# Kernel tuning notes

Hardware: AMD Instinct MI355X
Metric: run time of the kernel (lower is better)

The kernel has to match this reference:

```python
import jax, jax.numpy as jnp
import numpy as np

N, E, F, HID, PC, HEADS = 100000, 1600000, 128, 128, 16, 4
RATIO = 0.8
NEG_SLOPE = 0.2
BIG_NEG = -1e9


def setup_inputs() -> dict:
    ks = jax.random.split(jax.random.key(0), 20)
    def g(k, shape, fan):
        return jax.random.normal(k, shape, jnp.float32) / np.float32(np.sqrt(fan))
    return {
        "x": jax.random.normal(ks[0], (N, F), jnp.float32),
        "edge_index": jax.random.randint(ks[1], (2, E), 0, N, dtype=jnp.int32),
        "edge_attr": jax.random.uniform(ks[2], (E, 1), dtype=jnp.float32),
        "W1": g(ks[3], (F, PC), F),
        "att_src1": g(ks[4], (HEADS, PC // HEADS), PC // HEADS),
        "att_dst1": g(ks[5], (HEADS, PC // HEADS), PC // HEADS),
        "We1": g(ks[6], (1, PC), 1),
        "att_edge1": g(ks[7], (HEADS, PC // HEADS), PC // HEADS),
        "b1": jnp.zeros((PC,), jnp.float32),
        "Wrel": g(ks[8], (PC, 1), PC),
        "brel": jnp.zeros((1,), jnp.float32),
        "Wroot": g(ks[9], (PC, 1), PC),
        "W2": g(ks[10], (PC, HID), PC),
        "att_src2": g(ks[11], (1, HID), HID),
        "att_dst2": g(ks[12], (1, HID), HID),
        "We2": g(ks[13], (1, HID), 1),
        "att_edge2": g(ks[14], (1, HID), HID),
        "b2": jnp.zeros((HID,), jnp.float32),
        "Wg": g(ks[15], (HID, 1), HID),
        "bg": jnp.zeros((1,), jnp.float32),
    }


def gat_conv(h_in, src, dst, e_attr, W, a_s, a_d, We, a_e, b, num_nodes, mask=None):
    """PyG GATConv (add_self_loops=False, eval-mode so dropout is identity)."""
    H, D = a_s.shape
    h = (h_in @ W).reshape(-1, H, D)                      # [N,H,D]
    al_s = jnp.einsum('nhd,hd->nh', h, a_s)               # alpha contribution of source
    al_d = jnp.einsum('nhd,hd->nh', h, a_d)               # alpha contribution of dest
    he = (e_attr @ We).reshape(-1, H, D)                  # [E,H,D] edge features
    al_e = jnp.einsum('ehd,hd->eh', he, a_e)              # [E,H]
    logits = jax.nn.leaky_relu(al_s[src] + al_d[dst] + al_e, NEG_SLOPE)  # [E,H]
    if mask is not None:
        logits = jnp.where(mask[:, None], logits, BIG_NEG)
    # segment softmax over incoming edges of each destination node
    m = jnp.maximum(jax.ops.segment_max(logits, dst, num_segments=num_nodes), BIG_NEG)
    num = jnp.exp(logits - m[dst])
    if mask is not None:
        num = jnp.where(mask[:, None], num, 0.0)
    den = jax.ops.segment_sum(num, dst, num_segments=num_nodes)
    coef = num / jnp.maximum(den[dst], 1e-16)             # [E,H]
    out = jax.ops.segment_sum(coef[:, :, None] * h[src], dst, num_segments=num_nodes)
    return out.reshape(num_nodes, H * D) + b


def _forward(x, edge_attr, W1, att_src1, att_dst1, We1, att_edge1, b1,
             Wrel, brel, Wroot, W2, att_src2, att_dst2, We2, att_edge2, b2,
             Wg, bg, edge_index):
    n = x.shape[0]
    src, dst = edge_index[0], edge_index[1]
    h1 = jax.nn.relu(gat_conv(x, src, dst, edge_attr, W1, att_src1, att_dst1, We1, att_edge1, b1, n))
    # --- SAGPooling: GraphConv score -> tanh -> top-k -> masked subgraph (n > node_threshold always) ---
    agg = jax.ops.segment_sum(h1[src], dst, num_segments=n)           # neighbor sum
    score = (agg @ Wrel + brel + h1 @ Wroot).reshape(-1)              # GraphConv(16 -> 1)
    k = int(np.ceil(RATIO * n))                                       # static
    vals, perm = jax.lax.top_k(score, k)
    new_idx = jnp.full((n,), -1, dtype=jnp.int32).at[perm].set(jnp.arange(k, dtype=jnp.int32))
    src_n, dst_n = new_idx[src], new_idx[dst]
    emask = (src_n >= 0) & (dst_n >= 0)                               # edges with both ends kept
    src2 = jnp.where(emask, src_n, 0)
    dst2 = jnp.where(emask, dst_n, 0)
    x2 = h1[perm] * jnp.tanh(vals)[:, None]                           # gate kept nodes
    h2 = jax.nn.relu(gat_conv(x2, src2, dst2, edge_attr, W2, att_src2, att_dst2, We2, att_edge2, b2, k, mask=emask))
    # --- AttentionalAggregation + MaxAggregation over the single graph (index = zeros) ---
    gate = jax.nn.softmax(h2 @ Wg + bg, axis=0)                       # [k,1]
    att = (gate * h2).sum(axis=0, keepdims=True)                      # [1,HID]
    mx = h2.max(axis=0, keepdims=True)                                # [1,HID]
    return jnp.concatenate([att, mx], axis=1)                         # [1,2*HID]


def reference(x, edge_index, edge_attr, W1, att_src1, att_dst1, We1, att_edge1, b1,
              Wrel, brel, Wroot, W2, att_src2, att_dst2, We2, att_edge2, b2, Wg, bg):
    return _forward(x, edge_attr, W1, att_src1, att_dst1, We1, att_edge1, b1,
                    Wrel, brel, Wroot, W2, att_src2, att_dst2, We2, att_edge2, b2,
                    Wg, bg, edge_index)
```

## Files before the change

kernel.cpp:

```cpp
#include <hip/hip_runtime.h>
#include <hip/hip_bf16.h>

#define Nn 100000
#define Ee 1600000
#define Kk 80000
#define NB ((Nn + 255) / 256)
#define NBK 196
#define CHK 8192
#define G2B 2048

typedef unsigned int uint;
typedef unsigned short ushort;

struct Scal {
    uint prefix, remaining, needEq;
    float c1[4];
    float c2;
    uint gmaxOrd;
    float deng;
    float attnum[128];
    uint mxOrd[128];
};

__device__ __forceinline__ uint f2ord(float f) {
    uint b = __float_as_uint(f);
    return (b & 0x80000000u) ? ~b : (b | 0x80000000u);
}
__device__ __forceinline__ float ord2f(uint u) {
    uint b = (u & 0x80000000u) ? (u ^ 0x80000000u) : ~u;
    return __uint_as_float(b);
}
__device__ __forceinline__ float lrelu(float v) { return v > 0.f ? v : 0.2f * v; }
__device__ __forceinline__ float2 bf2f2(uint u) {
    return make_float2(__uint_as_float(u << 16), __uint_as_float(u & 0xFFFF0000u));
}

__global__ __launch_bounds__(256) void initK(uint* bcnt, uint* hist, Scal* sc,
                                             const float* We1, const float* ae1,
                                             const float* We2, const float* ae2) {
    int i = blockIdx.x * 256 + threadIdx.x;
    if (i < NBK) bcnt[i] = 0u;
    if (i < 256) hist[i] = 0u;
    if (i == 0) {
        sc->prefix = 0u; sc->remaining = Kk; sc->needEq = 0u;
        for (int h = 0; h < 4; h++) {
            float s = 0.f;
            for (int d = 0; d < 4; d++) s += We1[h * 4 + d] * ae1[h * 4 + d];
            sc->c1[h] = s;
        }
        float s2 = 0.f;
        for (int d = 0; d < 128; d++) s2 += We2[d] * ae2[d];
        sc->c2 = s2;
    }
}

__global__ __launch_bounds__(256) void nodeL1(const float* __restrict__ x,
                                              const float* __restrict__ W1,
                                              const float* __restrict__ as1,
                                              const float* __restrict__ ad1,
                                              float* __restrict__ hpre,
                                              float* __restrict__ alS1,
                                              float* __restrict__ alD1) {
    __shared__ float Ws[128 * 16];
    __shared__ float s_as[16], s_ad[16];
    for (int i = threadIdx.x; i < 2048; i += 256) Ws[i] = W1[i];
    if (threadIdx.x < 16) { s_as[threadIdx.x] = as1[threadIdx.x]; s_ad[threadIdx.x] = ad1[threadIdx.x]; }
    __syncthreads();
    int n = blockIdx.x * 256 + threadIdx.x;
    if (n >= Nn) return;
    float acc[16];
#pragma unroll
    for (int j = 0; j < 16; j++) acc[j] = 0.f;
    const float4* xr = (const float4*)(x + (size_t)n * 128);
    for (int t4 = 0; t4 < 32; t4++) {
        float4 xv = xr[t4];
#pragma unroll
        for (int j = 0; j < 16; j++) {
            acc[j] += xv.x * Ws[(t4 * 4 + 0) * 16 + j];
            acc[j] += xv.y * Ws[(t4 * 4 + 1) * 16 + j];
            acc[j] += xv.z * Ws[(t4 * 4 + 2) * 16 + j];
            acc[j] += xv.w * Ws[(t4 * 4 + 3) * 16 + j];
        }
    }
    float* hp = hpre + (size_t)n * 16;
#pragma unroll
    for (int j = 0; j < 16; j++) hp[j] = acc[j];
#pragma unroll
    for (int h = 0; h < 4; h++) {
        float s = 0.f, d = 0.f;
#pragma unroll
        for (int q = 0; q < 4; q++) {
            s += acc[h * 4 + q] * s_as[h * 4 + q];
            d += acc[h * 4 + q] * s_ad[h * 4 + q];
        }
        alS1[n * 4 + h] = s;
        alD1[n * 4 + h] = d;
    }
}

__global__ __launch_bounds__(256) void bucketCnt(const int* __restrict__ ei, uint* __restrict__ bcnt) {
    __shared__ uint h[NBK];
    if (threadIdx.x < NBK) h[threadIdx.x] = 0u;
    __syncthreads();
    for (int e = blockIdx.x * 256 + threadIdx.x; e < Ee; e += gridDim.x * 256)
        atomicAdd(&h[((uint)ei[Ee + e]) >> 9], 1u);
    __syncthreads();
    if (threadIdx.x < NBK && h[threadIdx.x]) atomicAdd(&bcnt[threadIdx.x], h[threadIdx.x]);
}

__global__ __launch_bounds__(256) void scanBk(const uint* __restrict__ bcnt, uint* __restrict__ boff,
                                              uint* __restrict__ gcur) {
    __shared__ uint s[256];
    int t = threadIdx.x;
    uint v = (t < NBK) ? bcnt[t] : 0u;
    s[t] = v;
    __syncthreads();
    for (int off = 1; off < 256; off <<= 1) {
        uint u = (t >= off) ? s[t - off] : 0u;
        __syncthreads();
        s[t] += u;
        __syncthreads();
    }
    if (t < NBK) { boff[t] = s[t] - v; gcur[t] = 0u; }
    if (t == 0) boff[NBK] = Ee;
}

__global__ __launch_bounds__(256) void binScat(const int* __restrict__ ei, const float* __restrict__ ea,
                                               const uint* __restrict__ boff, uint* __restrict__ gcur,
                                               uint2* __restrict__ bsE, ushort* __restrict__ bsD) {
    __shared__ uint h[NBK], base[NBK], h2[NBK];
    int t = threadIdx.x;
    if (t < NBK) h[t] = 0u;
    __syncthreads();
    int estart = blockIdx.x * CHK;
    int eend = min(Ee, estart + CHK);
    for (int e = estart + t; e < eend; e += 256)
        atomicAdd(&h[((uint)ei[Ee + e]) >> 9], 1u);
    __syncthreads();
    if (t < NBK) { base[t] = atomicAdd(&gcur[t], h[t]); h2[t] = 0u; }
    __syncthreads();
    for (int e = estart + t; e < eend; e += 256) {
        uint d = (uint)ei[Ee + e];
        uint b = d >> 9;
        uint r = atomicAdd(&h2[b], 1u);
        uint pos = boff[b] + base[b] + r;
        bsE[pos] = make_uint2((uint)ei[e], __float_as_uint(ea[e]));
        bsD[pos] = (ushort)(d & 511u);
    }
}

__global__ __launch_bounds__(256) void rankPlace(const uint* __restrict__ boff, const uint2* __restrict__ bsE,
                                                 const ushort* __restrict__ bsD,
                                                 uint2* __restrict__ csr_p8, uint* __restrict__ rowstart) {
    __shared__ uint ldeg[512];
    __shared__ uint lscan[512];
    __shared__ uint ps[256];
    int b = blockIdx.x, t = threadIdx.x;
    ldeg[t] = 0u; ldeg[t + 256] = 0u;
    __syncthreads();
    uint r0 = boff[b], r1 = boff[b + 1];
    for (uint i = r0 + t; i < r1; i += 256)
        atomicAdd(&ldeg[bsD[i]], 1u);
    __syncthreads();
    uint pv = ldeg[2 * t] + ldeg[2 * t + 1];
    ps[t] = pv;
    __syncthreads();
    for (int off = 1; off < 256; off <<= 1) {
        uint u = (t >= off) ? ps[t - off] : 0u;
        __syncthreads();
        ps[t] += u;
        __syncthreads();
    }
    uint pbase = ps[t] - pv;
    lscan[2 * t] = pbase;
    lscan[2 * t + 1] = pbase + ldeg[2 * t];
    __syncthreads();
    uint bb = boff[b];
    int nd = b * 512 + t;
    if (nd < Nn) rowstart[nd] = bb + lscan[t];
    nd = b * 512 + 256 + t;
    if (nd < Nn) rowstart[nd] = bb + lscan[256 + t];
    if (b == 0 && t == 0) rowstart[Nn] = Ee;
    ldeg[t] = 0u; ldeg[t + 256] = 0u;
    __syncthreads();
    for (uint i = r0 + t; i < r1; i += 256) {
        ushort dl = bsD[i];
        uint r = atomicAdd(&ldeg[dl], 1u);
        csr_p8[bb + lscan[dl] + r] = bsE[i];
    }
}

__global__ __launch_bounds__(256) void gather1f(const uint2* __restrict__ csr_p8,
                                                const uint* __restrict__ rowstart,
                                                const float* __restrict__ alS1, const float* __restrict__ alD1,
                                                const float* __restrict__ hpre, const Scal* __restrict__ scc,
                                                const float* __restrict__ b1, const float* __restrict__ Wrel,
                                                const float* __restrict__ Wroot,
                                                float* __restrict__ h1, float* __restrict__ p,
                                                float* __restrict__ q) {
    int tid = blockIdx.x * 256 + threadIdx.x;
    if (tid >= Nn * 4) return;
    int d = tid >> 2, h = tid & 3;
    uint r0 = rowstart[d], r1 = rowstart[d + 1];
    float ad = alD1[tid];
    float c1h = scc->c1[h];
    float den = 0.f;
    float4 acc = {0.f, 0.f, 0.f, 0.f};
#pragma unroll 8
    for (uint i = r0; i < r1; i++) {
        uint2 p8 = csr_p8[i];
        int s = (int)p8.x;
        float e = __expf(lrelu(alS1[s * 4 + h] + __uint_as_float(p8.y) * c1h + ad));
        float4 hv = *(const float4*)(hpre + (size_t)s * 16 + h * 4);
        den += e;
        acc.x += e * hv.x; acc.y += e * hv.y;
        acc.z += e * hv.z; acc.w += e * hv.w;
    }
    float inv = 1.f / fmaxf(den, 1e-16f);
    float4 o;
    o.x = fmaxf(acc.x * inv + b1[h * 4 + 0], 0.f);
    o.y = fmaxf(acc.y * inv + b1[h * 4 + 1], 0.f);
    o.z = fmaxf(acc.z * inv + b1[h * 4 + 2], 0.f);
    o.w = fmaxf(acc.w * inv + b1[h * 4 + 3], 0.f);
    *(float4*)(h1 + (size_t)d * 16 + h * 4) = o;
    float pp = o.x * Wrel[h * 4 + 0] + o.y * Wrel[h * 4 + 1] + o.z * Wrel[h * 4 + 2] + o.w * Wrel[h * 4 + 3];
    float qq = o.x * Wroot[h * 4 + 0] + o.y * Wroot[h * 4 + 1] + o.z * Wroot[h * 4 + 2] + o.w * Wroot[h * 4 + 3];
    pp += __shfl_xor(pp, 1); pp += __shfl_xor(pp, 2);
    qq += __shfl_xor(qq, 1); qq += __shfl_xor(qq, 2);
    if (h == 0) { p[d] = pp; q[d] = qq; }
}

__global__ __launch_bounds__(256) void scoreH(const uint2* __restrict__ csr_p8, const uint* __restrict__ rowstart,
                                              const float* __restrict__ p, const float* __restrict__ q,
                                              const float* __restrict__ brel,
                                              float* __restrict__ score, uint* __restrict__ dkey,
                                              uint* __restrict__ hist) {
    __shared__ uint lh[256];
    lh[threadIdx.x] = 0u;
    __syncthreads();
    int d = blockIdx.x * 256 + threadIdx.x;
    if (d < Nn) {
        uint r0 = rowstart[d], r1 = rowstart[d + 1];
        float s = brel[0] + q[d];
#pragma unroll 8
        for (uint i = r0; i < r1; i++) s += p[(int)csr_p8[i].x];
        score[d] = s;
        uint k = ~f2ord(s);
        dkey[d] = k;
        atomicAdd(&lh[k >> 24], 1u);
    }
    __syncthreads();
    if (lh[threadIdx.x]) atomicAdd(&hist[threadIdx.x], lh[threadIdx.x]);
}

__global__ __launch_bounds__(256) void histK(const uint* __restrict__ dkey, const Scal* __restrict__ sc,
                                             uint* __restrict__ hist, int shift) {
    __shared__ uint lh[256];
    lh[threadIdx.x] = 0u;
    __syncthreads();
    int i = blockIdx.x * 256 + threadIdx.x;
    if (i < Nn) {
        uint d = dkey[i];
        if ((d >> (shift + 8)) == sc->prefix) atomicAdd(&lh[(d >> shift) & 255u], 1u);
    }
    __syncthreads();
    if (lh[threadIdx.x]) atomicAdd(&hist[threadIdx.x], lh[threadIdx.x]);
}

__global__ __launch_bounds__(256) void selP(Scal* sc, uint* hist) {
    __shared__ uint s[256];
    int t = threadIdx.x;
    uint c = hist[t];
    s[t] = c;
    __syncthreads();
    for (int off = 1; off < 256; off <<= 1) {
        uint v = (t >= off) ? s[t - off] : 0u;
        __syncthreads();
        s[t] += v;
        __syncthreads();
    }
    uint rem = sc->remaining;
    uint cum = s[t];
    uint cumex = cum - c;
    if (cum >= rem && cumex < rem) {
        sc->remaining = rem - cumex;
        sc->prefix = (sc->prefix << 8) | (uint)t;
    }
    hist[t] = 0u;
}

__global__ __launch_bounds__(256) void cntK(const uint* __restrict__ dkey, const Scal* __restrict__ sc,
                                            uint* __restrict__ blkLt, uint* __restrict__ blkEq) {
    int i = blockIdx.x * 256 + threadIdx.x;
    uint ut = sc->prefix;
    bool lt = (i < Nn) && (dkey[i] < ut);
    bool eq = (i < Nn) && (dkey[i] == ut);
    __shared__ uint sl[4], se[4];
    unsigned long long bl = __ballot(lt), be = __ballot(eq);
    int lane = threadIdx.x & 63, w = threadIdx.x >> 6;
    if (lane == 0) { sl[w] = (uint)__popcll(bl); se[w] = (uint)__popcll(be); }
    __syncthreads();
    if (threadIdx.x == 0) {
        blkLt[blockIdx.x] = sl[0] + sl[1] + sl[2] + sl[3];
        blkEq[blockIdx.x] = se[0] + se[1] + se[2] + se[3];
    }
}

__global__ __launch_bounds__(512) void prefP(Scal* sc, const uint* __restrict__ blkLt,
                                             const uint* __restrict__ blkEq, uint* __restrict__ eqPref) {
    __shared__ uint se[512];
    __shared__ uint sl[512];
    int t = threadIdx.x;
    uint e = (t < NB) ? blkEq[t] : 0u;
    uint l = (t < NB) ? blkLt[t] : 0u;
    se[t] = e; sl[t] = l;
    __syncthreads();
    for (int off = 1; off < 512; off <<= 1) {
        uint v1 = (t >= off) ? se[t - off] : 0u;
        uint v2 = (t >= off) ? sl[t - off] : 0u;
        __syncthreads();
        se[t] += v1; sl[t] += v2;
        __syncthreads();
    }
    if (t < NB) eqPref[t] = se[t] - e;
    if (t == 511) sc->needEq = Kk - sl[511];
}

__global__ __launch_bounds__(256) void keptK(const uint* __restrict__ dkey, const Scal* __restrict__ sc,
                                             const uint* __restrict__ eqPref, int* __restrict__ kept) {
    int i = blockIdx.x * 256 + threadIdx.x;
    uint ut = sc->prefix, needEq = sc->needEq;
    bool inr = i < Nn;
    uint d = inr ? dkey[i] : 0xFFFFFFFFu;
    bool isLt = inr && (d < ut);
    bool isEq = inr && (d == ut);
    __shared__ uint wcnt[4];
    unsigned long long mask = __ballot(isEq);
    int lane = threadIdx.x & 63, w = threadIdx.x >> 6;
    uint lanePre = (uint)__popcll(mask & ((1ull << lane) - 1ull));
    if (lane == 0) wcnt[w] = (uint)__popcll(mask);
    __syncthreads();
    uint wo = 0;
    for (int qq = 0; qq < 4; qq++) if (qq < w) wo += wcnt[qq];
    uint rank = eqPref[blockIdx.x] + wo + lanePre;
    if (inr) kept[i] = (isLt || (isEq && rank < needEq)) ? 1 : 0;
}

__global__ __launch_bounds__(256) void nodeL2(const float* __restrict__ h1, const float* __restrict__ score,
                                              const int* __restrict__ kept, const float* __restrict__ W2,
                                              const float* __restrict__ as2, const float* __restrict__ ad2,
                                              __hip_bfloat162* __restrict__ h2b, float* __restrict__ alS2k,
                                              float* __restrict__ alD2) {
    __shared__ float Ws[16 * 128];
    for (int i = threadIdx.x; i < 2048; i += 256) Ws[i] = W2[i];
    __syncthreads();
    int wid = (blockIdx.x * 256 + threadIdx.x) >> 6;
    int lane = threadIdx.x & 63;
    if (wid >= Nn) return;
    int n = wid;
    if (!kept[n]) { if (lane == 0) alS2k[n] = -1e30f; return; }
    float t = tanhf(score[n]);
    float x2[16];
    const float* hr = h1 + (size_t)n * 16;
#pragma unroll
    for (int j = 0; j < 16; j++) x2[j] = hr[j] * t;
    int d0 = 2 * lane, d1 = 2 * lane + 1;
    float a0 = 0.f, a1 = 0.f;
    const float2* Wv = (const float2*)Ws;
#pragma unroll
    for (int j = 0; j < 16; j++) {
        float2 wv = Wv[j * 64 + lane];
        a0 += x2[j] * wv.x;
        a1 += x2[j] * wv.y;
    }
    __hip_bfloat162 hb;
    hb.x = __float2bfloat16(a0);
    hb.y = __float2bfloat16(a1);
    h2b[(size_t)n * 64 + lane] = hb;
    float s = a0 * as2[d0] + a1 * as2[d1];
    float dd = a0 * ad2[d0] + a1 * ad2[d1];
#pragma unroll
    for (int off = 32; off; off >>= 1) { s += __shfl_xor(s, off); dd += __shfl_xor(dd, off); }
    if (lane == 0) { alS2k[n] = s; alD2[n] = dd; }
}

__global__ __launch_bounds__(256) void gather2h(const uint2* __restrict__ csr_p8,
                                                const uint* __restrict__ rowstart,
                                                const float* __restrict__ alS2k, const float* __restrict__ alD2,
                                                const Scal* __restrict__ scc,
                                                const __hip_bfloat162* __restrict__ h2b, const float* __restrict__ b2,
                                                const float* __restrict__ Wg, const float* __restrict__ bg,
                                                float* __restrict__ pacc, float* __restrict__ pmx,
                                                float* __restrict__ pden) {
    __shared__ float sAtt[4][16][8];
    __shared__ float sMx[4][16][8];
    __shared__ float sDen[4];
    int w = threadIdx.x >> 6, lane = threadIdx.x & 63;
    int g = lane >> 4, t = lane & 15;
    float4 b2a = ((const float4*)b2)[t * 2], b2b = ((const float4*)b2)[t * 2 + 1];
    float4 wga = ((const float4*)Wg)[t * 2], wgb = ((const float4*)Wg)[t * 2 + 1];
    float bg0 = bg[0];
    float c2 = scc->c2;
    const uint* h2u = (const uint*)h2b;
    float att[8], mx8[8], denP = 0.f;
#pragma unroll
    for (int j = 0; j < 8; j++) { att[j] = 0.f; mx8[j] = 0.f; }
    for (int n = blockIdx.x * 4 + w; n < Nn; n += G2B * 4) {
        float sk = alS2k[n];
        if (sk <= -1e29f) continue;
        float ad = alD2[n];
        uint r0 = rowstart[n];
        uint len = rowstart[n + 1] - r0;
        float den = 0.f;
        float acc[8];
#pragma unroll
        for (int d = 0; d < 8; d++) acc[d] = 0.f;
#pragma unroll 2
        for (uint base = 0; base < len; base += 4) {
            float cmy = 0.f;
            int smy = 0;
            if (lane < 4) {
                uint off = base + (uint)lane;
                if (off < len) {
                    uint2 p8 = csr_p8[r0 + off];
                    smy = (int)p8.x;
                    float pv = alS2k[smy] + __uint_as_float(p8.y) * c2;
                    cmy = __expf(lrelu(pv + ad));
                }
            }
            float c = __shfl(cmy, g);
            int s = __shfl(smy, g);
            uint4 hv = *(const uint4*)(h2u + (size_t)s * 64 + t * 4);
            den += c;
            float2 f;
            f = bf2f2(hv.x); acc[0] += c * f.x; acc[1] += c * f.y;
            f = bf2f2(hv.y); acc[2] += c * f.x; acc[3] += c * f.y;
            f = bf2f2(hv.z); acc[4] += c * f.x; acc[5] += c * f.y;
            f = bf2f2(hv.w); acc[6] += c * f.x; acc[7] += c * f.y;
        }
#pragma unroll
        for (int d = 0; d < 8; d++) {
            acc[d] += __shfl_xor(acc[d], 16);
            acc[d] += __shfl_xor(acc[d], 32);
        }
        den += __shfl_xor(den, 16);
        den += __shfl_xor(den, 32);
        float inv = 1.f / fmaxf(den, 1e-16f);
        float o[8];
        o[0] = fmaxf(acc[0] * inv + b2a.x, 0.f);
        o[1] = fmaxf(acc[1] * inv + b2a.y, 0.f);
        o[2] = fmaxf(acc[2] * inv + b2a.z, 0.f);
        o[3] = fmaxf(acc[3] * inv + b2a.w, 0.f);
        o[4] = fmaxf(acc[4] * inv + b2b.x, 0.f);
        o[5] = fmaxf(acc[5] * inv + b2b.y, 0.f);
        o[6] = fmaxf(acc[6] * inv + b2b.z, 0.f);
        o[7] = fmaxf(acc[7] * inv + b2b.w, 0.f);
        float gp = o[0] * wga.x + o[1] * wga.y + o[2] * wga.z + o[3] * wga.w +
                   o[4] * wgb.x + o[5] * wgb.y + o[6] * wgb.z + o[7] * wgb.w;
#pragma unroll
        for (int off = 8; off; off >>= 1) gp += __shfl_xor(gp, off);
        float e = __expf(gp + bg0);
        denP += e;
#pragma unroll
        for (int j = 0; j < 8; j++) {
            att[j] += e * o[j];
            mx8[j] = fmaxf(mx8[j], o[j]);
        }
    }
    if (g == 0) {
#pragma unroll
        for (int j = 0; j < 8; j++) { sAtt[w][t][j] = att[j]; sMx[w][t][j] = mx8[j]; }
    }
    if (lane == 0) sDen[w] = denP;
    __syncthreads();
    int tid = threadIdx.x;
    if (tid < 128) {
        int tt = tid >> 3, j = tid & 7;
        float a = sAtt[0][tt][j] + sAtt[1][tt][j] + sAtt[2][tt][j] + sAtt[3][tt][j];
        float m = fmaxf(fmaxf(sMx[0][tt][j], sMx[1][tt][j]), fmaxf(sMx[2][tt][j], sMx[3][tt][j]));
        pacc[(size_t)blockIdx.x * 128 + tid] = a;
        pmx[(size_t)blockIdx.x * 128 + tid] = m;
    }
    if (tid == 0) pden[blockIdx.x] = sDen[0] + sDen[1] + sDen[2] + sDen[3];
}

__global__ __launch_bounds__(256) void gateOut(const float* __restrict__ pacc, const float* __restrict__ pmx,
                                               const float* __restrict__ pden, float* __restrict__ out) {
    __shared__ float r[256];
    __shared__ float rd[256];
    int b = blockIdx.x, tid = threadIdx.x;
    float a = 0.f, m = 0.f, dsum = 0.f;
    for (int i = tid; i < G2B; i += 256) {
        a += pacc[(size_t)i * 128 + b];
        m = fmaxf(m, pmx[(size_t)i * 128 + b]);
        dsum += pden[i];
    }
    r[tid] = a; rd[tid] = dsum;
    __syncthreads();
    for (int off = 128; off; off >>= 1) {
        if (tid < off) { r[tid] += r[tid + off]; rd[tid] += rd[tid + off]; }
        __syncthreads();
    }
    float asum = r[0], deng = rd[0];
    __syncthreads();
    r[tid] = m;
    __syncthreads();
    for (int off = 128; off; off >>= 1) {
        if (tid < off) r[tid] = fmaxf(r[tid], r[tid + off]);
        __syncthreads();
    }
    if (tid == 0) {
        out[b] = asum / deng;
        out[128 + b] = r[0];
    }
}

extern "C" void kernel_launch(void* const* d_in, const int* in_sizes, int n_in,
                              void* d_out, int out_size, void* d_ws, size_t ws_size,
                              hipStream_t stream) {
    const float* x = (const float*)d_in[0];
    const int* ei = (const int*)d_in[1];
    const float* ea = (const float*)d_in[2];
    const float* W1 = (const float*)d_in[3];
    const float* as1 = (const float*)d_in[4];
    const float* ad1 = (const float*)d_in[5];
    const float* We1 = (const float*)d_in[6];
    const float* ae1 = (const float*)d_in[7];
    const float* b1 = (const float*)d_in[8];
    const float* Wrel = (const float*)d_in[9];
    const float* brel = (const float*)d_in[10];
    const float* Wroot = (const float*)d_in[11];
    const float* W2 = (const float*)d_in[12];
    const float* as2 = (const float*)d_in[13];
    const float* ad2 = (const float*)d_in[14];
    const float* We2 = (const float*)d_in[15];
    const float* ae2 = (const float*)d_in[16];
    const float* b2 = (const float*)d_in[17];
    const float* Wg = (const float*)d_in[18];
    const float* bg = (const float*)d_in[19];
    float* out = (float*)d_out;

    float* base = (float*)d_ws;
    size_t o = 0;
    auto alloc = [&](size_t nf) { float* p2 = base + o; o += nf; return p2; };
    uint2* bsE = (uint2*)alloc((size_t)Ee * 2);
    ushort* bsD = (ushort*)alloc((size_t)Ee / 2);
    uint2* csr_p8 = (uint2*)alloc((size_t)Ee * 2);
    __hip_bfloat162* h2b = (__hip_bfloat162*)alloc((size_t)Nn * 64);
    float* hpre = alloc((size_t)Nn * 16);
    float* h1 = alloc((size_t)Nn * 16);
    float* pacc = alloc((size_t)G2B * 128);
    float* pmx = alloc((size_t)G2B * 128);
    float* pden = alloc(G2B);
    float* alS1 = alloc((size_t)Nn * 4);
    float* alD1 = alloc((size_t)Nn * 4);
    float* p = alloc(Nn);
    float* q = alloc(Nn);
    float* score = alloc(Nn);
    uint* dkey = (uint*)alloc(Nn);
    int* kept = (int*)alloc(Nn);
    float* alS2k = alloc(Nn);
    float* alD2 = alloc(Nn);
    uint* rowstart = (uint*)alloc(Nn + 1);
    uint* hist = (uint*)alloc(256);
    uint* blkLt = (uint*)alloc(NB);
    uint* blkEq = (uint*)alloc(NB);
    uint* eqPref = (uint*)alloc(NB);
    uint* bcnt = (uint*)alloc(NBK);
    uint* boff = (uint*)alloc(NBK + 1);
    uint* gcur = (uint*)alloc(NBK);
    Scal* sc = (Scal*)alloc(512);

    auto cdiv = [](long a, long b) { return (int)((a + b - 1) / b); };

    initK<<<NB, 256, 0, stream>>>(bcnt, hist, sc, We1, ae1, We2, ae2);
    nodeL1<<<NB, 256, 0, stream>>>(x, W1, as1, ad1, hpre, alS1, alD1);
    bucketCnt<<<512, 256, 0, stream>>>(ei, bcnt);
    scanBk<<<1, 256, 0, stream>>>(bcnt, boff, gcur);
    binScat<<<cdiv(Ee, CHK), 256, 0, stream>>>(ei, ea, boff, gcur, bsE, bsD);
    rankPlace<<<NBK, 256, 0, stream>>>(boff, bsE, bsD, csr_p8, rowstart);
    gather1f<<<cdiv((long)Nn * 4, 256), 256, 0, stream>>>(csr_p8, rowstart, alS1, alD1, hpre, sc,
                                                          b1, Wrel, Wroot, h1, p, q);
    scoreH<<<NB, 256, 0, stream>>>(csr_p8, rowstart, p, q, brel, score, dkey, hist);
    selP<<<1, 256, 0, stream>>>(sc, hist);
    for (int shift = 16; shift >= 0; shift -= 8) {
        histK<<<NB, 256, 0, stream>>>(dkey, sc, hist, shift);
        selP<<<1, 256, 0, stream>>>(sc, hist);
    }
    cntK<<<NB, 256, 0, stream>>>(dkey, sc, blkLt, blkEq);
    prefP<<<1, 512, 0, stream>>>(sc, blkLt, blkEq, eqPref);
    keptK<<<NB, 256, 0, stream>>>(dkey, sc, eqPref, kept);
    nodeL2<<<cdiv(Nn, 4), 256, 0, stream>>>(h1, score, kept, W2, as2, ad2, h2b, alS2k, alD2);
    gather2h<<<G2B, 256, 0, stream>>>(csr_p8, rowstart, alS2k, alD2, sc,
                                      h2b, b2, Wg, bg, pacc, pmx, pden);
    gateOut<<<128, 256, 0, stream>>>(pacc, pmx, pden, out);
}
```

Measured before the change: 335.5 us.

## Fuse radix top-k selection into one single-block kernel; compute edge weights per group in gather2

Replaces the chain of histogram, select, count, prefix and keep kernels for top-k with one 1024-thread single-block kernel. That kernel runs three more radix passes over all node keys and then a sequential ranked scan to mark kept nodes. This removes about ten kernel launches and their global round-trips, but a single workgroup now streams 100k keys four times. Separately, gather2 now has every lane compute its group's edge coefficient directly instead of four lanes computing and shuffling, and the unroll goes from 2 to 4.

```diff
diff --git a/kernel.cpp b/kernel.cpp
--- a/kernel.cpp
+++ b/kernel.cpp
@@ -13,22 +13,13 @@
 typedef unsigned short ushort;
 
 struct Scal {
-    uint prefix, remaining, needEq;
     float c1[4];
     float c2;
-    uint gmaxOrd;
-    float deng;
-    float attnum[128];
-    uint mxOrd[128];
 };
 
 __device__ __forceinline__ uint f2ord(float f) {
     uint b = __float_as_uint(f);
     return (b & 0x80000000u) ? ~b : (b | 0x80000000u);
-}
-__device__ __forceinline__ float ord2f(uint u) {
-    uint b = (u & 0x80000000u) ? (u ^ 0x80000000u) : ~u;
-    return __uint_as_float(b);
 }
 __device__ __forceinline__ float lrelu(float v) { return v > 0.f ? v : 0.2f * v; }
 __device__ __forceinline__ float2 bf2f2(uint u) {
@@ -42,7 +33,6 @@
     if (i < NBK) bcnt[i] = 0u;
     if (i < 256) hist[i] = 0u;
     if (i == 0) {
-        sc->prefix = 0u; sc->remaining = Kk; sc->needEq = 0u;
         for (int h = 0; h < 4; h++) {
             float s = 0.f;
             for (int d = 0; d < 4; d++) s += We1[h * 4 + d] * ae1[h * 4 + d];
@@ -253,97 +243,68 @@
     if (lh[threadIdx.x]) atomicAdd(&hist[threadIdx.x], lh[threadIdx.x]);
 }
 
-__global__ __launch_bounds__(256) void histK(const uint* __restrict__ dkey, const Scal* __restrict__ sc,
-                                             uint* __restrict__ hist, int shift) {
-    __shared__ uint lh[256];
-    lh[threadIdx.x] = 0u;
-    __syncthreads();
-    int i = blockIdx.x * 256 + threadIdx.x;
-    if (i < Nn) {
-        uint d = dkey[i];
-        if ((d >> (shift + 8)) == sc->prefix) atomicAdd(&lh[(d >> shift) & 255u], 1u);
-    }
-    __syncthreads();
-    if (lh[threadIdx.x]) atomicAdd(&hist[threadIdx.x], lh[threadIdx.x]);
-}
-
-__global__ __launch_bounds__(256) void selP(Scal* sc, uint* hist) {
-    __shared__ uint s[256];
+__global__ __launch_bounds__(1024) void topk1b(const uint* __restrict__ dkey, const uint* __restrict__ hist,
+                                               int* __restrict__ kept) {
+    __shared__ uint sh[256];
+    __shared__ uint s_prefix, s_rem, s_eqbase;
+    __shared__ uint wcnt[16];
     int t = threadIdx.x;
-    uint c = hist[t];
-    s[t] = c;
-    __syncthreads();
-    for (int off = 1; off < 256; off <<= 1) {
-        uint v = (t >= off) ? s[t - off] : 0u;
-        __syncthreads();
-        s[t] += v;
-        __syncthreads();
-    }
-    uint rem = sc->remaining;
-    uint cum = s[t];
-    uint cumex = cum - c;
-    if (cum >= rem && cumex < rem) {
-        sc->remaining = rem - cumex;
-        sc->prefix = (sc->prefix << 8) | (uint)t;
-    }
-    hist[t] = 0u;
-}
-
-__global__ __launch_bounds__(256) void cntK(const uint* __restrict__ dkey, const Scal* __restrict__ sc,
-                                            uint* __restrict__ blkLt, uint* __restrict__ blkEq) {
-    int i = blockIdx.x * 256 + threadIdx.x;
-    uint ut = sc->prefix;
-    bool lt = (i < Nn) && (dkey[i] < ut);
-    bool eq = (i < Nn) && (dkey[i] == ut);
-    __shared__ uint sl[4], se[4];
-    unsigned long long bl = __ballot(lt), be = __ballot(eq);
-    int lane = threadIdx.x & 63, w = threadIdx.x >> 6;
-    if (lane == 0) { sl[w] = (uint)__popcll(bl); se[w] = (uint)__popcll(be); }
-    __syncthreads();
-    if (threadIdx.x == 0) {
-        blkLt[blockIdx.x] = sl[0] + sl[1] + sl[2] + sl[3];
-        blkEq[blockIdx.x] = se[0] + se[1] + se[2] + se[3];
-    }
-}
-
-__global__ __launch_bounds__(512) void prefP(Scal* sc, const uint* __restrict__ blkLt,
-                                             const uint* __restrict__ blkEq, uint* __restrict__ eqPref) {
-    __shared__ uint se[512];
-    __shared__ uint sl[512];
-    int t = threadIdx.x;
-    uint e = (t < NB) ? blkEq[t] : 0u;
-    uint l = (t < NB) ? blkLt[t] : 0u;
-    se[t] = e; sl[t] = l;
-    __syncthreads();
-    for (int off = 1; off < 512; off <<= 1) {
-        uint v1 = (t >= off) ? se[t - off] : 0u;
-        uint v2 = (t >= off) ? sl[t - off] : 0u;
-        __syncthreads();
-        se[t] += v1; sl[t] += v2;
-        __syncthreads();
-    }
-    if (t < NB) eqPref[t] = se[t] - e;
-    if (t == 511) sc->needEq = Kk - sl[511];
-}
-
-__global__ __launch_bounds__(256) void keptK(const uint* __restrict__ dkey, const Scal* __restrict__ sc,
-                                             const uint* __restrict__ eqPref, int* __restrict__ kept) {
-    int i = blockIdx.x * 256 + threadIdx.x;
-    uint ut = sc->prefix, needEq = sc->needEq;
-    bool inr = i < Nn;
-    uint d = inr ? dkey[i] : 0xFFFFFFFFu;
-    bool isLt = inr && (d < ut);
-    bool isEq = inr && (d == ut);
-    __shared__ uint wcnt[4];
-    unsigned long long mask = __ballot(isEq);
-    int lane = threadIdx.x & 63, w = threadIdx.x >> 6;
-    uint lanePre = (uint)__popcll(mask & ((1ull << lane) - 1ull));
-    if (lane == 0) wcnt[w] = (uint)__popcll(mask);
-    __syncthreads();
-    uint wo = 0;
-    for (int qq = 0; qq < 4; qq++) if (qq < w) wo += wcnt[qq];
-    uint rank = eqPref[blockIdx.x] + wo + lanePre;
-    if (inr) kept[i] = (isLt || (isEq && rank < needEq)) ? 1 : 0;
+    if (t == 0) { s_prefix = 0u; s_rem = Kk; s_eqbase = 0u; }
+    if (t < 256) sh[t] = hist[t];
+    __syncthreads();
+    for (int lvl = 0; lvl < 4; lvl++) {
+        if (lvl > 0) {
+            int shift = 24 - 8 * lvl;
+            if (t < 256) sh[t] = 0u;
+            uint pref = s_prefix;
+            __syncthreads();
+            for (int i = t; i < Nn; i += 1024) {
+                uint d = dkey[i];
+                if ((d >> (shift + 8)) == pref) atomicAdd(&sh[(d >> shift) & 255u], 1u);
+            }
+            __syncthreads();
+        }
+        uint c = (t < 256) ? sh[t] : 0u;
+        for (int off = 1; off < 256; off <<= 1) {
+            uint u = (t < 256 && t >= off) ? sh[t - off] : 0u;
+            __syncthreads();
+            if (t < 256) sh[t] += u;
+            __syncthreads();
+        }
+        uint rem = s_rem;
+        if (t < 256) {
+            uint cum = sh[t], cumex = cum - c;
+            if (cum >= rem && cumex < rem) {
+                s_rem = rem - cumex;
+                s_prefix = (s_prefix << 8) | (uint)t;
+            }
+        }
+        __syncthreads();
+    }
+    uint ut = s_prefix, needEq = s_rem;
+    int lane = t & 63, w = t >> 6;
+    for (int baseI = 0; baseI < Nn; baseI += 1024) {
+        __syncthreads();
+        uint eqb = s_eqbase;
+        int i = baseI + t;
+        bool valid = i < Nn;
+        uint d = valid ? dkey[i] : 0xFFFFFFFFu;
+        bool isLt = valid && (d < ut);
+        bool isEq = valid && (d == ut);
+        unsigned long long mask = __ballot(isEq);
+        uint lanePre = (uint)__popcll(mask & ((1ull << lane) - 1ull));
+        if (lane == 0) wcnt[w] = (uint)__popcll(mask);
+        __syncthreads();
+        uint wo = 0;
+        for (int k = 0; k < w; k++) wo += wcnt[k];
+        uint rank = eqb + wo + lanePre;
+        if (valid) kept[i] = (isLt || (isEq && rank < needEq)) ? 1 : 0;
+        if (t == 0) {
+            uint tot = 0;
+            for (int k = 0; k < 16; k++) tot += wcnt[k];
+            s_eqbase = eqb + tot;
+        }
+    }
 }
 
 __global__ __launch_bounds__(256) void nodeL2(const float* __restrict__ h1, const float* __restrict__ score,
@@ -384,7 +345,7 @@
     if (lane == 0) { alS2k[n] = s; alD2[n] = dd; }
 }
 
-__global__ __launch_bounds__(256) void gather2h(const uint2* __restrict__ csr_p8,
+__global__ __launch_bounds__(256) void gather2g(const uint2* __restrict__ csr_p8,
                                                 const uint* __restrict__ rowstart,
                                                 const float* __restrict__ alS2k, const float* __restrict__ alD2,
                                                 const Scal* __restrict__ scc,
@@ -415,21 +376,16 @@
         float acc[8];
 #pragma unroll
         for (int d = 0; d < 8; d++) acc[d] = 0.f;
-#pragma unroll 2
+#pragma unroll 4
         for (uint base = 0; base < len; base += 4) {
-            float cmy = 0.f;
-            int smy = 0;
-            if (lane < 4) {
-                uint off = base + (uint)lane;
-                if (off < len) {
-                    uint2 p8 = csr_p8[r0 + off];
-                    smy = (int)p8.x;
-                    float pv = alS2k[smy] + __uint_as_float(p8.y) * c2;
-                    cmy = __expf(lrelu(pv + ad));
-                }
-            }
-            float c = __shfl(cmy, g);
-            int s = __shfl(smy, g);
+            uint off = base + (uint)g;
+            bool act = off < len;
+            uint sidx = act ? (r0 + off) : (r0 + len - 1);
+            uint2 p8 = csr_p8[sidx];
+            int s = (int)p8.x;
+            float pv = alS2k[s] + __uint_as_float(p8.y) * c2;
+            pv = act ? pv : -1e30f;
+            float c = __expf(lrelu(pv + ad));
             uint4 hv = *(const uint4*)(h2u + (size_t)s * 64 + t * 4);
             den += c;
             float2 f;
@@ -563,13 +519,10 @@
     float* alD2 = alloc(Nn);
     uint* rowstart = (uint*)alloc(Nn + 1);
     uint* hist = (uint*)alloc(256);
-    uint* blkLt = (uint*)alloc(NB);
-    uint* blkEq = (uint*)alloc(NB);
-    uint* eqPref = (uint*)alloc(NB);
     uint* bcnt = (uint*)alloc(NBK);
     uint* boff = (uint*)alloc(NBK + 1);
     uint* gcur = (uint*)alloc(NBK);
-    Scal* sc = (Scal*)alloc(512);
+    Scal* sc = (Scal*)alloc(64);
 
     auto cdiv = [](long a, long b) { return (int)((a + b - 1) / b); };
 
@@ -582,16 +535,9 @@
     gather1f<<<cdiv((long)Nn * 4, 256), 256, 0, stream>>>(csr_p8, rowstart, alS1, alD1, hpre, sc,
                                                           b1, Wrel, Wroot, h1, p, q);
     scoreH<<<NB, 256, 0, stream>>>(csr_p8, rowstart, p, q, brel, score, dkey, hist);
-    selP<<<1, 256, 0, stream>>>(sc, hist);
-    for (int shift = 16; shift >= 0; shift -= 8) {
-        histK<<<NB, 256, 0, stream>>>(dkey, sc, hist, shift);
-        selP<<<1, 256, 0, stream>>>(sc, hist);
-    }
-    cntK<<<NB, 256, 0, stream>>>(dkey, sc, blkLt, blkEq);
-    prefP<<<1, 512, 0, stream>>>(sc, blkLt, blkEq, eqPref);
-    keptK<<<NB, 256, 0, stream>>>(dkey, sc, eqPref, kept);
+    topk1b<<<1, 1024, 0, stream>>>(dkey, hist, kept);
     nodeL2<<<cdiv(Nn, 4), 256, 0, stream>>>(h1, score, kept, W2, as2, ad2, h2b, alS2k, alD2);
-    gather2h<<<G2B, 256, 0, stream>>>(csr_p8, rowstart, alS2k, alD2, sc,
+    gather2g<<<G2B, 256, 0, stream>>>(csr_p8, rowstart, alS2k, alD2, sc,
                                       h2b, b2, Wg, bg, pacc, pmx, pden);
     gateOut<<<128, 256, 0, stream>>>(pacc, pmx, pden, out);
 }
```

Result: slower. 439.8 us (+31.1%).
